# Kernel optimization log

Hardware: AMD Instinct MI355X
Metric: run time of the kernel (lower is better)

Reference implementation:

```python
import jax, jax.numpy as jnp
import numpy as np

HEADS = 16
HEAD_DIM = 128


def rotate_half(x):
    x1, x2 = x[..., : x.shape[-1] // 2], x[..., x.shape[-1] // 2 :]
    return jnp.concatenate((-x2, x1), axis=-1)


def setup_inputs() -> dict:
    key = jax.random.key(0)
    ks = jax.random.split(key, 8)
    b, s, h = 2, 2048, 2048
    d = HEAD_DIM
    sc = 1.0 / np.sqrt(h)
    x = jax.random.normal(ks[0], (b, s, h), jnp.float32)
    # real RoPE angles for realism
    inv_freq = 1.0 / (10000.0 ** (jnp.arange(0, d, 2, dtype=jnp.float32) / d))
    t = jnp.arange(s, dtype=jnp.float32)
    freqs = jnp.outer(t, inv_freq)  # [s, d/2]
    emb = jnp.concatenate((freqs, freqs), axis=-1)  # [s, d]
    return {
        "x": x,
        "cos": jnp.cos(emb),
        "sin": jnp.sin(emb),
        "wq": jax.random.normal(ks[1], (h, h), jnp.float32) * sc,
        "bq": jnp.zeros((h,), jnp.float32),
        "wk": jax.random.normal(ks[2], (h, h), jnp.float32) * sc,
        "bk": jnp.zeros((h,), jnp.float32),
        "wv": jax.random.normal(ks[3], (h, h), jnp.float32) * sc,
        "bv": jnp.zeros((h,), jnp.float32),
        "wo": jax.random.normal(ks[4], (h, h), jnp.float32) * sc,
    }


def reference(x, cos, sin, wq, bq, wk, bk, wv, bv, wo):
    b, s, hidden = x.shape
    nh, d = HEADS, HEAD_DIM
    # QKV projections (F.linear: x @ W.T + b)
    def split_heads(t):
        return t.reshape(b, s, nh, d).transpose(0, 2, 1, 3)  # [b,h,s,d]
    q = split_heads(x @ wq.T + bq)
    k = split_heads(x @ wk.T + bk)
    v = split_heads(x @ wv.T + bv)
    # RoPE (cos/sin: [s,d] broadcast over [b,h,s,d])
    q = q * cos + rotate_half(q) * sin
    k = k * cos + rotate_half(k) * sin
    # full (non-causal) attention, materializing [b,h,s,s] scores as original
    scale = 1.0 / jnp.sqrt(jnp.asarray(d, x.dtype))
    scores = jnp.einsum("bhqd,bhkd->bhqk", q, k) * scale
    attn = jax.nn.softmax(scores, axis=-1)
    out = jnp.einsum("bhqk,bhkd->bhqd", attn, v)  # [b,h,s,d]
    out = out.transpose(0, 2, 1, 3).reshape(b, s, hidden)
    # o_proj: no bias
    return out @ wo.T
```

## Files before the change

kernel.cpp:

```cpp
#include <hip/hip_runtime.h>

#define B_  2
#define NH  16
#define S_  2048
#define D_  128
#define HID 2048

typedef _Float16 half_t;
typedef _Float16 f16x8 __attribute__((ext_vector_type(8)));
typedef _Float16 f16x4_t __attribute__((ext_vector_type(4)));
typedef float f32x4 __attribute__((ext_vector_type(4)));

__device__ __forceinline__ void glds16(const half_t* g, half_t* l) {
    __builtin_amdgcn_global_load_lds(
        (const __attribute__((address_space(1))) void*)g,
        (__attribute__((address_space(3))) void*)l, 16, 0, 0);
}
__device__ __forceinline__ float fexp2(float x) { return __builtin_amdgcn_exp2f(x); }

__global__ __launch_bounds__(256) void cvt_all(
    const float* __restrict__ x,  const float* __restrict__ wq, const float* __restrict__ wk,
    const float* __restrict__ wv, const float* __restrict__ wo, half_t* __restrict__ dst)
{
    long i = ((long)blockIdx.x * 256 + threadIdx.x) * 4;
    const float* src; long off;
    if (i < 8388608)       { src = x;  off = i; }
    else if (i < 12582912) { src = wq; off = i - 8388608; }
    else if (i < 16777216) { src = wk; off = i - 12582912; }
    else if (i < 20971520) { src = wv; off = i - 16777216; }
    else                   { src = wo; off = i - 20971520; }
    float4 v = *(const float4*)(src + off);
    f16x4_t h;
    h[0] = (half_t)v.x; h[1] = (half_t)v.y; h[2] = (half_t)v.z; h[3] = (half_t)v.w;
    *(f16x4_t*)(dst + i) = h;
}

__global__ __launch_bounds__(256, 3) void qkv_gemm(
    const half_t* __restrict__ xb,
    const half_t* __restrict__ wqb, const half_t* __restrict__ wkb, const half_t* __restrict__ wvb,
    const float* __restrict__ bq, const float* __restrict__ bk, const float* __restrict__ bv,
    const float* __restrict__ cosp, const float* __restrict__ sinp,
    half_t* __restrict__ qo, half_t* __restrict__ ko, half_t* __restrict__ vto)
{
    __shared__ __align__(16) half_t As[128 * 64];
    __shared__ __align__(16) half_t Bs[128 * 64];
    const int m0 = blockIdx.x * 128;
    const int n0 = blockIdx.y * 128;
    const int z  = blockIdx.z;
    const half_t* wb   = (z == 0) ? wqb : (z == 1) ? wkb : wvb;
    const float*  bias = (z == 0) ? bq  : (z == 1) ? bk  : bv;
    const int tid = threadIdx.x, wave = tid >> 6, lane = tid & 63;
    const int quad = lane >> 4, lrow = lane & 15;
    const int wm = wave >> 1, wn = wave & 1;

    const int sr = wave * 8 + (lane >> 3);
    const int c8 = ((lane & 7) - (lane >> 3)) & 7;
    const half_t* ag = xb + (size_t)(m0 + sr) * HID + c8 * 8;
    const half_t* bg = wb + (size_t)(n0 + sr) * HID + c8 * 8;
    half_t* alb = &As[(wave * 8) * 64];
    half_t* blb = &Bs[(wave * 8) * 64];

    f32x4 acc[4][4] = {};

    for (int k0 = 0; k0 < HID; k0 += 64) {
        __syncthreads();
#pragma unroll
        for (int p = 0; p < 4; ++p) {
            glds16(ag + k0 + (size_t)(p * 32) * HID, alb + p * 32 * 64);
            glds16(bg + k0 + (size_t)(p * 32) * HID, blb + p * 32 * 64);
        }
        __syncthreads();
#pragma unroll
        for (int ks = 0; ks < 2; ++ks) {
            f16x8 af[4], bf[4];
#pragma unroll
            for (int mt = 0; mt < 4; mt++) {
                const int ra = wm * 64 + mt * 16 + lrow;
                const int pa = (ks * 4 + quad + (ra & 7)) & 7;
                af[mt] = *(const f16x8*)&As[ra * 64 + pa * 8];
            }
#pragma unroll
            for (int nt = 0; nt < 4; nt++) {
                const int rb = wn * 16 + nt * 32 + lrow;
                const int pb = (ks * 4 + quad + (rb & 7)) & 7;
                bf[nt] = *(const f16x8*)&Bs[rb * 64 + pb * 8];
            }
#pragma unroll
            for (int mt = 0; mt < 4; mt++)
#pragma unroll
                for (int nt = 0; nt < 4; nt++)
                    acc[mt][nt] = __builtin_amdgcn_mfma_f32_16x16x32_f16(af[mt], bf[nt], acc[mt][nt], 0, 0, 0);
        }
    }

    const int head = blockIdx.y;
    float bs_[4];
#pragma unroll
    for (int nt = 0; nt < 4; nt++) bs_[nt] = bias[n0 + nt * 32 + wn * 16 + lrow];
#pragma unroll
    for (int mt = 0; mt < 4; mt++) {
#pragma unroll
        for (int r = 0; r < 4; r++) {
            const int m  = m0 + wm * 64 + mt * 16 + quad * 4 + r;
            const int bb = m >> 11;
            const int st = m & (S_ - 1);
            float res[4];
#pragma unroll
            for (int nt = 0; nt < 4; nt++) res[nt] = acc[mt][nt][r] + bs_[nt];
            if (z < 2) {
                const float* cr = cosp + st * D_;
                const float* sr2 = sinp + st * D_;
#pragma unroll
                for (int pr = 0; pr < 2; pr++) {
                    const int dlo = pr * 32 + wn * 16 + lrow;
                    float cl = cr[dlo], sl = sr2[dlo], ch = cr[dlo + 64], sh = sr2[dlo + 64];
                    float lo = res[pr], hi = res[pr + 2];
                    res[pr]     = lo * cl - hi * sl;
                    res[pr + 2] = hi * ch + lo * sh;
                }
                half_t* dst = (z == 0 ? qo : ko) + ((size_t)(bb * NH + head) * S_ + st) * D_;
#pragma unroll
                for (int nt = 0; nt < 4; nt++) dst[nt * 32 + wn * 16 + lrow] = (half_t)res[nt];
            } else {
                half_t* dst = vto + (size_t)(bb * NH + head) * D_ * S_ + st;
#pragma unroll
                for (int nt = 0; nt < 4; nt++) dst[(size_t)(nt * 32 + wn * 16 + lrow) * S_] = (half_t)res[nt];
            }
        }
    }
}

#define PLD 72
__global__ __launch_bounds__(256, 2) void attn_kernel(
    const half_t* __restrict__ qb, const half_t* __restrict__ kb,
    const half_t* __restrict__ vtb, half_t* __restrict__ ob)
{
    __shared__ __align__(16) half_t ks[64 * 128];
    __shared__ __align__(16) half_t vs[128 * 64];
    __shared__ __align__(16) half_t ps[4 * 32 * PLD];
    const int head = blockIdx.y, b = blockIdx.z;
    const int bh = b * NH + head;
    const int tid = threadIdx.x, wave = tid >> 6, lane = tid & 63;
    const int quad = lane >> 4, lrow = lane & 15;
    const float SC = 0.08838834764831845f * 1.4426950408889634f;
    const int q0 = blockIdx.x * 128 + wave * 32;

    f16x8 qf[2][4];
#pragma unroll
    for (int mt = 0; mt < 2; mt++) {
        const half_t* qrow = qb + ((size_t)bh * S_ + q0 + mt * 16 + lrow) * D_;
#pragma unroll
        for (int kc = 0; kc < 4; kc++) {
            f16x8 v = *(const f16x8*)(qrow + kc * 32 + quad * 8);
#pragma unroll
            for (int j = 0; j < 8; j++) v[j] = (half_t)((float)v[j] * SC);
            qf[mt][kc] = v;
        }
    }

    const half_t* kbase = kb + (size_t)bh * S_ * D_;
    const half_t* vbase = vtb + (size_t)bh * D_ * S_;
    const int pbase = wave * 32 * PLD;

    f16x8 kreg[4], vreg[4];
#define LOAD_TILE(kt_) do {                                                           \
    _Pragma("unroll")                                                                 \
    for (int i = 0; i < 4; i++) {                                                     \
        const int rk_ = wave * 16 + i * 4 + (lane >> 4);                              \
        const int ck_ = (((lane & 15) - (rk_ & 7)) & 15) * 8;                         \
        kreg[i] = *(const f16x8*)(kbase + (size_t)((kt_) * 64 + rk_) * D_ + ck_);     \
        const int rv_ = wave * 32 + i * 8 + (lane >> 3);                              \
        const int cv_ = (((lane & 7) - (rv_ & 7)) & 7) * 8;                           \
        vreg[i] = *(const f16x8*)(vbase + (size_t)rv_ * S_ + (kt_) * 64 + cv_);       \
    }                                                                                 \
} while (0)
#define WRITE_TILE() do {                                                             \
    _Pragma("unroll")                                                                 \
    for (int i = 0; i < 4; i++) {                                                     \
        *(f16x8*)&ks[(wave * 16 + i * 4) * 128 + lane * 8] = kreg[i];                 \
        *(f16x8*)&vs[(wave * 32 + i * 8) * 64  + lane * 8] = vreg[i];                 \
    }                                                                                 \
} while (0)

    float m_run[2] = {-1e30f, -1e30f}, l_run[2] = {0.f, 0.f};
    f32x4 o[2][8] = {};

    LOAD_TILE(0);
    WRITE_TILE();
    __syncthreads();

    for (int kt = 0; kt < 32; kt++) {
        if (kt + 1 < 32) LOAD_TILE(kt + 1);

        f32x4 st[2][4] = {};
        __builtin_amdgcn_s_setprio(1);
#pragma unroll
        for (int nt = 0; nt < 4; nt++) {
            const int rk2 = nt * 16 + lrow;
#pragma unroll
            for (int kc = 0; kc < 4; kc++) {
                const int pk = (kc * 4 + quad + (rk2 & 7)) & 15;
                f16x8 kf = *(const f16x8*)&ks[rk2 * 128 + pk * 8];
                st[0][nt] = __builtin_amdgcn_mfma_f32_16x16x32_f16(kf, qf[0][kc], st[0][nt], 0, 0, 0);
                st[1][nt] = __builtin_amdgcn_mfma_f32_16x16x32_f16(kf, qf[1][kc], st[1][nt], 0, 0, 0);
            }
        }
        __builtin_amdgcn_s_setprio(0);

        bool upd = false;
        float alpha[2];
#pragma unroll
        for (int mt = 0; mt < 2; mt++) {
            float m01 = fmaxf(fmaxf(st[mt][0][0], st[mt][0][1]), fmaxf(st[mt][0][2], st[mt][0][3]));
            float m11 = fmaxf(fmaxf(st[mt][1][0], st[mt][1][1]), fmaxf(st[mt][1][2], st[mt][1][3]));
            float m21 = fmaxf(fmaxf(st[mt][2][0], st[mt][2][1]), fmaxf(st[mt][2][2], st[mt][2][3]));
            float m31 = fmaxf(fmaxf(st[mt][3][0], st[mt][3][1]), fmaxf(st[mt][3][2], st[mt][3][3]));
            float mx = fmaxf(fmaxf(m01, m11), fmaxf(m21, m31));
            mx = fmaxf(mx, __shfl_xor(mx, 16));
            mx = fmaxf(mx, __shfl_xor(mx, 32));
            const float mnew = fmaxf(m_run[mt], mx);
            alpha[mt] = fexp2(m_run[mt] - mnew);
            upd = upd || (mnew > m_run[mt]);
            m_run[mt] = mnew;
            float rs = 0.f;
#pragma unroll
            for (int nt = 0; nt < 4; nt++) {
                f16x4_t pk4;
#pragma unroll
                for (int r = 0; r < 4; r++) {
                    float p = fexp2(st[mt][nt][r] - mnew);
                    rs += p;
                    pk4[r] = (half_t)p;
                }
                *(f16x4_t*)&ps[pbase + (mt * 16 + lrow) * PLD + nt * 16 + quad * 4] = pk4;
            }
            rs += __shfl_xor(rs, 16);
            rs += __shfl_xor(rs, 32);
            l_run[mt] = l_run[mt] * alpha[mt] + rs;
        }
        if (__any(upd)) {
#pragma unroll
            for (int mt = 0; mt < 2; mt++) {
                float ab[4];
#pragma unroll
                for (int r = 0; r < 4; r++) ab[r] = __shfl(alpha[mt], quad * 4 + r, 16);
#pragma unroll
                for (int dt = 0; dt < 8; dt++)
#pragma unroll
                    for (int r = 0; r < 4; r++) o[mt][dt][r] *= ab[r];
            }
        }

        __builtin_amdgcn_s_setprio(1);
#pragma unroll
        for (int kc2 = 0; kc2 < 2; kc2++) {
            f16x8 pf0 = *(const f16x8*)&ps[pbase + lrow * PLD + kc2 * 32 + quad * 8];
            f16x8 pf1 = *(const f16x8*)&ps[pbase + (16 + lrow) * PLD + kc2 * 32 + quad * 8];
#pragma unroll
            for (int dt = 0; dt < 8; dt++) {
                const int rv2 = dt * 16 + lrow;
                const int pv = (kc2 * 4 + quad + (rv2 & 7)) & 7;
                f16x8 vf = *(const f16x8*)&vs[rv2 * 64 + pv * 8];
                o[0][dt] = __builtin_amdgcn_mfma_f32_16x16x32_f16(pf0, vf, o[0][dt], 0, 0, 0);
                o[1][dt] = __builtin_amdgcn_mfma_f32_16x16x32_f16(pf1, vf, o[1][dt], 0, 0, 0);
            }
        }
        __builtin_amdgcn_s_setprio(0);

        __syncthreads();
        if (kt + 1 < 32) WRITE_TILE();
        __syncthreads();
    }

#pragma unroll
    for (int mt = 0; mt < 2; mt++) {
        const float rl = 1.f / l_run[mt];
        float rb[4];
#pragma unroll
        for (int r = 0; r < 4; r++) rb[r] = __shfl(rl, quad * 4 + r, 16);
#pragma unroll
        for (int dt = 0; dt < 8; dt++) {
            const int d = dt * 16 + lrow;
#pragma unroll
            for (int r = 0; r < 4; r++) {
                const int row = q0 + mt * 16 + quad * 4 + r;
                ob[((size_t)b * S_ + row) * HID + head * D_ + d] = (half_t)(o[mt][dt][r] * rb[r]);
            }
        }
    }
#undef LOAD_TILE
#undef WRITE_TILE
}

__global__ __launch_bounds__(256, 3) void out_gemm(
    const half_t* __restrict__ ab, const half_t* __restrict__ wob, float* __restrict__ out)
{
    __shared__ __align__(16) half_t As[128 * 64];
    __shared__ __align__(16) half_t Bs[128 * 64];
    const int m0 = blockIdx.x * 128;
    const int n0 = blockIdx.y * 128;
    const int tid = threadIdx.x, wave = tid >> 6, lane = tid & 63;
    const int quad = lane >> 4, lrow = lane & 15;
    const int wm = wave >> 1, wn = wave & 1;

    const int sr = wave * 8 + (lane >> 3);
    const int c8 = ((lane & 7) - (lane >> 3)) & 7;
    const half_t* ag = ab  + (size_t)(m0 + sr) * HID + c8 * 8;
    const half_t* bg = wob + (size_t)(n0 + sr) * HID + c8 * 8;
    half_t* alb = &As[(wave * 8) * 64];
    half_t* blb = &Bs[(wave * 8) * 64];

    f32x4 acc[4][4] = {};

    for (int k0 = 0; k0 < HID; k0 += 64) {
        __syncthreads();
#pragma unroll
        for (int p = 0; p < 4; ++p) {
            glds16(ag + k0 + (size_t)(p * 32) * HID, alb + p * 32 * 64);
            glds16(bg + k0 + (size_t)(p * 32) * HID, blb + p * 32 * 64);
        }
        __syncthreads();
#pragma unroll
        for (int ks = 0; ks < 2; ++ks) {
            f16x8 af[4], bf[4];
#pragma unroll
            for (int mt = 0; mt < 4; mt++) {
                const int ra = wm * 64 + mt * 16 + lrow;
                const int pa = (ks * 4 + quad + (ra & 7)) & 7;
                af[mt] = *(const f16x8*)&As[ra * 64 + pa * 8];
            }
#pragma unroll
            for (int nt = 0; nt < 4; nt++) {
                const int rb = wn * 16 + nt * 32 + lrow;
                const int pb = (ks * 4 + quad + (rb & 7)) & 7;
                bf[nt] = *(const f16x8*)&Bs[rb * 64 + pb * 8];
            }
#pragma unroll
            for (int mt = 0; mt < 4; mt++)
#pragma unroll
                for (int nt = 0; nt < 4; nt++)
                    acc[mt][nt] = __builtin_amdgcn_mfma_f32_16x16x32_f16(af[mt], bf[nt], acc[mt][nt], 0, 0, 0);
        }
    }

#pragma unroll
    for (int mt = 0; mt < 4; mt++)
#pragma unroll
        for (int r = 0; r < 4; r++) {
            const int m = m0 + wm * 64 + mt * 16 + quad * 4 + r;
#pragma unroll
            for (int nt = 0; nt < 4; nt++)
                out[(size_t)m * HID + n0 + nt * 32 + wn * 16 + lrow] = acc[mt][nt][r];
        }
}

extern "C" void kernel_launch(void* const* d_in, const int* in_sizes, int n_in,
                              void* d_out, int out_size, void* d_ws, size_t ws_size,
                              hipStream_t stream)
{
    const float* x    = (const float*)d_in[0];
    const float* cosp = (const float*)d_in[1];
    const float* sinp = (const float*)d_in[2];
    const float* wq   = (const float*)d_in[3];
    const float* bq   = (const float*)d_in[4];
    const float* wk   = (const float*)d_in[5];
    const float* bk   = (const float*)d_in[6];
    const float* wv   = (const float*)d_in[7];
    const float* bv   = (const float*)d_in[8];
    const float* wo   = (const float*)d_in[9];
    float* out = (float*)d_out;

    half_t* w   = (half_t*)d_ws;
    half_t* xb  = w;
    half_t* wqb = xb  + 8388608;
    half_t* wkb = wqb + 4194304;
    half_t* wvb = wkb + 4194304;
    half_t* wob = wvb + 4194304;
    half_t* qo  = wob + 4194304;
    half_t* ko  = qo  + 8388608;
    half_t* vto = ko  + 8388608;
    half_t* ob  = vto + 8388608;

    cvt_all<<<24576, 256, 0, stream>>>(x, wq, wk, wv, wo, xb);
    qkv_gemm<<<dim3(32, 16, 3), 256, 0, stream>>>(xb, wqb, wkb, wvb, bq, bk, bv,
                                                  cosp, sinp, qo, ko, vto);
    attn_kernel<<<dim3(16, 16, 2), 256, 0, stream>>>(qo, ko, vto, ob);
    out_gemm<<<dim3(32, 16), 256, 0, stream>>>(ob, wob, out);
}
```

Measured before the change: 414.0 us.

## Halve out-projection GEMM K-tile with new LDS swizzle; tree-reduce softmax row sums

The output-projection GEMM now stages K in 32-wide tiles instead of 64, which halves its LDS footprint. The global-to-LDS load mapping and XOR-style swizzle are redone for the narrower rows. The smaller footprint may allow more resident blocks per CU, but the K loop runs twice as many iterations with a pair of barriers each, so there is more sync overhead per unit of work. Separately, the attention softmax row-sum is restructured from a serial accumulation into a pairwise tree to shorten the dependency chain.

```diff
diff --git a/kernel.cpp b/kernel.cpp
--- a/kernel.cpp
+++ b/kernel.cpp
@@ -222,18 +222,20 @@
             alpha[mt] = fexp2(m_run[mt] - mnew);
             upd = upd || (mnew > m_run[mt]);
             m_run[mt] = mnew;
-            float rs = 0.f;
+            float rsp[4];
 #pragma unroll
             for (int nt = 0; nt < 4; nt++) {
                 f16x4_t pk4;
-#pragma unroll
-                for (int r = 0; r < 4; r++) {
-                    float p = fexp2(st[mt][nt][r] - mnew);
-                    rs += p;
-                    pk4[r] = (half_t)p;
-                }
+                float r0 = fexp2(st[mt][nt][0] - mnew);
+                float r1 = fexp2(st[mt][nt][1] - mnew);
+                float r2 = fexp2(st[mt][nt][2] - mnew);
+                float r3 = fexp2(st[mt][nt][3] - mnew);
+                pk4[0] = (half_t)r0; pk4[1] = (half_t)r1;
+                pk4[2] = (half_t)r2; pk4[3] = (half_t)r3;
+                rsp[nt] = (r0 + r1) + (r2 + r3);
                 *(f16x4_t*)&ps[pbase + (mt * 16 + lrow) * PLD + nt * 16 + quad * 4] = pk4;
             }
+            float rs = (rsp[0] + rsp[1]) + (rsp[2] + rsp[3]);
             rs += __shfl_xor(rs, 16);
             rs += __shfl_xor(rs, 32);
             l_run[mt] = l_run[mt] * alpha[mt] + rs;
@@ -295,52 +297,54 @@
 __global__ __launch_bounds__(256, 3) void out_gemm(
     const half_t* __restrict__ ab, const half_t* __restrict__ wob, float* __restrict__ out)
 {
-    __shared__ __align__(16) half_t As[128 * 64];
-    __shared__ __align__(16) half_t Bs[128 * 64];
+    __shared__ __align__(16) half_t As[128 * 32];
+    __shared__ __align__(16) half_t Bs[128 * 32];
     const int m0 = blockIdx.x * 128;
     const int n0 = blockIdx.y * 128;
     const int tid = threadIdx.x, wave = tid >> 6, lane = tid & 63;
     const int quad = lane >> 4, lrow = lane & 15;
     const int wm = wave >> 1, wn = wave & 1;
 
-    const int sr = wave * 8 + (lane >> 3);
-    const int c8 = ((lane & 7) - (lane >> 3)) & 7;
-    const half_t* ag = ab  + (size_t)(m0 + sr) * HID + c8 * 8;
-    const half_t* bg = wob + (size_t)(n0 + sr) * HID + c8 * 8;
-    half_t* alb = &As[(wave * 8) * 64];
-    half_t* blb = &Bs[(wave * 8) * 64];
+    const int r0 = wave * 32 + (lane >> 2);
+    const int r1 = r0 + 16;
+    const int c0 = (((lane & 3) - (r0 >> 1)) & 3) * 8;
+    const int c1 = (((lane & 3) - (r1 >> 1)) & 3) * 8;
+    const half_t* ag0 = ab  + (size_t)(m0 + r0) * HID + c0;
+    const half_t* ag1 = ab  + (size_t)(m0 + r1) * HID + c1;
+    const half_t* bg0 = wob + (size_t)(n0 + r0) * HID + c0;
+    const half_t* bg1 = wob + (size_t)(n0 + r1) * HID + c1;
+    half_t* al0 = &As[(wave * 32) * 32];
+    half_t* al1 = &As[(wave * 32 + 16) * 32];
+    half_t* bl0 = &Bs[(wave * 32) * 32];
+    half_t* bl1 = &Bs[(wave * 32 + 16) * 32];
 
     f32x4 acc[4][4] = {};
 
-    for (int k0 = 0; k0 < HID; k0 += 64) {
-        __syncthreads();
-#pragma unroll
-        for (int p = 0; p < 4; ++p) {
-            glds16(ag + k0 + (size_t)(p * 32) * HID, alb + p * 32 * 64);
-            glds16(bg + k0 + (size_t)(p * 32) * HID, blb + p * 32 * 64);
-        }
-        __syncthreads();
-#pragma unroll
-        for (int ks = 0; ks < 2; ++ks) {
-            f16x8 af[4], bf[4];
-#pragma unroll
-            for (int mt = 0; mt < 4; mt++) {
-                const int ra = wm * 64 + mt * 16 + lrow;
-                const int pa = (ks * 4 + quad + (ra & 7)) & 7;
-                af[mt] = *(const f16x8*)&As[ra * 64 + pa * 8];
-            }
-#pragma unroll
-            for (int nt = 0; nt < 4; nt++) {
-                const int rb = wn * 16 + nt * 32 + lrow;
-                const int pb = (ks * 4 + quad + (rb & 7)) & 7;
-                bf[nt] = *(const f16x8*)&Bs[rb * 64 + pb * 8];
-            }
-#pragma unroll
-            for (int mt = 0; mt < 4; mt++)
-#pragma unroll
-                for (int nt = 0; nt < 4; nt++)
-                    acc[mt][nt] = __builtin_amdgcn_mfma_f32_16x16x32_f16(af[mt], bf[nt], acc[mt][nt], 0, 0, 0);
-        }
+    for (int k0 = 0; k0 < HID; k0 += 32) {
+        __syncthreads();
+        glds16(ag0 + k0, al0);
+        glds16(ag1 + k0, al1);
+        glds16(bg0 + k0, bl0);
+        glds16(bg1 + k0, bl1);
+        __syncthreads();
+        f16x8 af[4], bf[4];
+#pragma unroll
+        for (int mt = 0; mt < 4; mt++) {
+            const int ra = wm * 64 + mt * 16 + lrow;
+            const int pa = (quad + (ra >> 1)) & 3;
+            af[mt] = *(const f16x8*)&As[ra * 32 + pa * 8];
+        }
+#pragma unroll
+        for (int nt = 0; nt < 4; nt++) {
+            const int rb = wn * 16 + nt * 32 + lrow;
+            const int pb = (quad + (rb >> 1)) & 3;
+            bf[nt] = *(const f16x8*)&Bs[rb * 32 + pb * 8];
+        }
+#pragma unroll
+        for (int mt = 0; mt < 4; mt++)
+#pragma unroll
+            for (int nt = 0; nt < 4; nt++)
+                acc[mt][nt] = __builtin_amdgcn_mfma_f32_16x16x32_f16(af[mt], bf[nt], acc[mt][nt], 0, 0, 0);
     }
 
 #pragma unroll
```

Result: no change. 415.3 us, median of 2 (+0.3%).
